# Kernel tuning notes

Measured on AMD Instinct MI355X. Metric: run time of the kernel, lower is better.

Reference implementation:

```python
import jax, jax.numpy as jnp
import numpy as np

NMS_THRESH = 0.5
SCORE_THRESH = 0.05
MAX_DET = 300


def _iou_one_vs_all(box, boxes):
    # box: [4] (x1,y1,x2,y2); boxes: [N,4]
    x1 = jnp.maximum(box[0], boxes[:, 0])
    y1 = jnp.maximum(box[1], boxes[:, 1])
    x2 = jnp.minimum(box[2], boxes[:, 2])
    y2 = jnp.minimum(box[3], boxes[:, 3])
    inter = jnp.maximum(x2 - x1, 0.0) * jnp.maximum(y2 - y1, 0.0)
    area_a = (box[2] - box[0]) * (box[3] - box[1])
    area_b = (boxes[:, 2] - boxes[:, 0]) * (boxes[:, 3] - boxes[:, 1])
    union = area_a + area_b - inter
    return inter / jnp.maximum(union, 1e-8)


def _nms_single_class(boxes, scores):
    # Greedy NMS with max_output_size=MAX_DET, matching tf.image.non_max_suppression
    # after score-threshold prefiltering. boxes:[N,4], scores:[N].
    s0 = jnp.where(scores > SCORE_THRESH, scores, -jnp.inf)

    def step(s, _):
        i = jnp.argmax(s)
        si = s[i]
        sel = jnp.isfinite(si)  # False once no candidates remain
        iou = _iou_one_vs_all(boxes[i], boxes)
        s = jnp.where(sel & (iou > NMS_THRESH), -jnp.inf, s)
        s = s.at[i].set(-jnp.inf)
        return s, (i, si, sel)

    _, (idx, sv, sel) = jax.lax.scan(step, s0, None, length=MAX_DET)
    # unselected slots carry -inf score
    return idx.astype(jnp.int32), jnp.where(sel, sv, -jnp.inf)


def _filter_one_image(boxes, classification, other):
    # boxes:[N,4], classification:[N,C], other:[N,D]
    C = classification.shape[1]
    # class-specific NMS (class_specific_filter=True, nms=True)
    idx, sv = jax.vmap(lambda c: _nms_single_class(boxes, classification[:, c]))(
        jnp.arange(C))  # each [C, MAX_DET]
    labels = jnp.broadcast_to(jnp.arange(C)[:, None], idx.shape)
    cand_scores = sv.reshape(-1)          # [C*MAX_DET]
    cand_idx = idx.reshape(-1)
    cand_lab = labels.reshape(-1)
    # global top-k over all per-class survivors
    top_s, top_i = jax.lax.top_k(cand_scores, MAX_DET)
    sel_idx = cand_idx[top_i]
    sel_lab = cand_lab[top_i]
    valid = jnp.isfinite(top_s)
    # pad invalid slots with -1 (matches tf.pad(..., constant_values=-1))
    out_boxes = jnp.where(valid[:, None], boxes[sel_idx], -1.0)
    out_scores = jnp.where(valid, top_s, -1.0)
    out_labels = jnp.where(valid, sel_lab, -1).astype(jnp.int32)
    out_other = jnp.where(valid[:, None], other[sel_idx], -1.0)
    return out_boxes, out_scores, out_labels, out_other


def setup_inputs() -> dict:
    key = jax.random.key(0)
    k1, k2, k3, k4 = jax.random.split(key, 4)
    B, N, C, D = 16, 50000, 8, 2
    xy = jax.random.uniform(k1, (B, N, 2), jnp.float32, 0.0, 512.0)
    wh = jax.random.uniform(k2, (B, N, 2), jnp.float32, 4.0, 100.0)
    boxes = jnp.concatenate([xy, xy + wh], axis=-1)  # valid (x1,y1,x2,y2)
    classification = jax.random.uniform(k3, (B, N, C), jnp.float32)
    other = jax.random.normal(k4, (B, N, D), jnp.float32)
    return {"boxes": boxes, "classification": classification, "other": other}


def reference(boxes, classification, other):
    # tf.map_fn over batch -> vmap over batch
    return jax.vmap(_filter_one_image)(boxes, classification, other)
```

## Files before the change

### kernel.cpp

```cpp
#include <hip/hip_runtime.h>
#include <math.h>
#include <stdint.h>

#define NB 16
#define NN 50000
#define NC 8
#define ND 2
#define MAX_DET 300
#define NMS_T 0.5f
#define SCORE_T 0.05f
#define CAP 1024
#define CUTBIN 252
#define LBUF 128
#define NTILE32 32
#define CHUNK 256
#define NT 1024
#define NPI (NN * NC)
#define F4PB (NPI / 4 / NTILE32)

typedef unsigned long long u64;

__device__ __forceinline__ float neg_inf() { return -__builtin_inff(); }

__device__ __forceinline__ bool iou_gt(float ax1, float ay1, float ax2, float ay2,
                                       float area_a,
                                       float bx1, float by1, float bx2, float by2,
                                       float area_b) {
    float x1 = fmaxf(ax1, bx1), y1 = fmaxf(ay1, by1);
    float x2 = fminf(ax2, bx2), y2 = fminf(ay2, by2);
    float inter = __fmul_rn(fmaxf(__fsub_rn(x2, x1), 0.0f),
                            fmaxf(__fsub_rn(y2, y1), 0.0f));
    float uni = __fsub_rn(__fadd_rn(area_a, area_b), inter);
    return inter > __fmul_rn(0.5f, fmaxf(uni, 1e-8f));
}

__device__ __forceinline__ u64 score_key(float s, int n) {
    unsigned u = __float_as_uint(s);
    u ^= (u & 0x80000000u) ? 0xFFFFFFFFu : 0x80000000u;
    return ((u64)u << 32) | (unsigned)(~(unsigned)n);
}

__device__ __forceinline__ u64 shfl_xor_u64(u64 v, int m) {
    unsigned lo = (unsigned)v, hi = (unsigned)(v >> 32);
    lo = __shfl_xor(lo, m, 64);
    hi = __shfl_xor(hi, m, 64);
    return ((u64)hi << 32) | lo;
}

__global__ __launch_bounds__(1024) void compact_kernel(
    const float* __restrict__ cls, int* __restrict__ tcnt_g,
    u64* __restrict__ cand)
{
    const int b = blockIdx.x >> 5, t32 = blockIdx.x & 31;
    const int tid = threadIdx.x;
    __shared__ u64 buf[8][LBUF];
    __shared__ int lcnt[8];
    if (tid < 8) lcnt[tid] = 0;
    __syncthreads();

    const float4* c4 = (const float4*)(cls + (size_t)b * NPI);
    const int f0 = t32 * F4PB, fend = f0 + F4PB;

    for (int f = f0 + tid; f < fend; f += 1024) {
        float4 v = c4[f];
        int cb = (f & 1) * 4;
        int n = f >> 1;
        float vv[4] = {v.x, v.y, v.z, v.w};
        #pragma unroll
        for (int k = 0; k < 4; ++k) {
            float s = vv[k];
            if (s > SCORE_T) {
                int bn = (int)(s * 256.0f); if (bn > 255) bn = 255;
                if (bn >= CUTBIN) {
                    int c = cb + k;
                    int pos = atomicAdd(&lcnt[c], 1);
                    if (pos < LBUF) buf[c][pos] = score_key(s, n);
                }
            }
        }
    }
    __syncthreads();
    {
        int c = tid >> 7, i = tid & (LBUF - 1);
        int m = lcnt[c];
        if (i < (m < LBUF ? m : LBUF))
            cand[(size_t)(((b * 8 + c) * NTILE32) + t32) * LBUF + i] = buf[c][i];
        if (i == 0) tcnt_g[(b * 8 + c) * NTILE32 + t32] = m;
    }
}

__global__ __launch_bounds__(NT) void nms_fused(
    const float* __restrict__ boxes, const float* __restrict__ cls,
    const u64* __restrict__ cand, const int* __restrict__ tcnt_g,
    int* __restrict__ sel_idx, float* __restrict__ sel_score)
{
    const int bc = blockIdx.x;
    const int b = bc >> 3, c = bc & 7;
    const int tid = threadIdx.x;
    const int lane = tid & 63;
    const float4* bx4 = (const float4*)(boxes + (size_t)b * NN * 4);
    const float* sr = cls + (size_t)b * NN * NC + c;
    int* si = sel_idx + bc * MAX_DET;
    float* ss = sel_score + bc * MAX_DET;

    __shared__ u64 keys[CAP];
    __shared__ int tcnt_s[NTILE32], toff_s[NTILE32];
    __shared__ int sh_total, sh_ovf;
    __shared__ u64 M64[4][CHUNK];
    __shared__ unsigned presup4[4][CHUNK];
    __shared__ float4 cbox2[2][CHUNK];
    __shared__ float  carea2[2][CHUNK];
    __shared__ int    cidx2[2][CHUNK];
    __shared__ float  cscore2[2][CHUNK];
    __shared__ u64 accs4_s[4];
    __shared__ float4 abox[MAX_DET];
    __shared__ float aarea[MAX_DET];
    __shared__ unsigned bm[(NN + 31) / 32];
    __shared__ float rv[NT];
    __shared__ int   ri[NT];
    __shared__ float sboxsh[5];

    if (tid < 64) {
        int v = (lane < NTILE32) ? tcnt_g[bc * NTILE32 + lane] : 0;
        int incl = v;
        #pragma unroll
        for (int d = 1; d < 32; d <<= 1) {
            int o = __shfl_up(incl, d, 64);
            if (lane >= d) incl += o;
        }
        if (lane < NTILE32) { tcnt_s[lane] = v; toff_s[lane] = incl - v; }
        u64 ov = __ballot(lane < NTILE32 && v > LBUF);
        if (lane == 31) { sh_total = incl; sh_ovf = (ov != 0); }
    }
    __syncthreads();
    const int cnt = sh_total;
    const bool full_fb = sh_ovf || (cnt > CAP);
    const int inSet = cnt < CAP ? cnt : CAP;

    int n_acc = 0;
    if (!full_fb) {
        for (int i = tid; i < CAP; i += NT) keys[i] = 0ull;
        __syncthreads();
        for (int s = tid; s < NTILE32 * LBUF; s += NT) {
            int t = s >> 7, i = s & (LBUF - 1);
            if (i < tcnt_s[t])
                keys[toff_s[t] + i] = cand[(size_t)(bc * NTILE32 + t) * LBUF + i];
        }
        __syncthreads();

        const int p0 = (tid >> 6) * 128 + lane, p1 = p0 + 64;
        u64 v0 = 0, v1 = 0;
        if (tid < 512) {
            v0 = keys[p0]; v1 = keys[p1];
            #pragma unroll
            for (int k = 2; k <= 128; k <<= 1) {
                #pragma unroll
                for (int j = k >> 1; j > 0; j >>= 1) {
                    if (j == 64) {
                        bool dir = ((p0 & k) == 0);
                        if ((v0 < v1) == dir) { u64 t = v0; v0 = v1; v1 = t; }
                    } else {
                        bool lower = ((lane & j) == 0);
                        bool dir0 = ((p0 & k) == 0);
                        bool dir1 = ((p1 & k) == 0);
                        u64 o0 = shfl_xor_u64(v0, j);
                        u64 mx0 = v0 > o0 ? v0 : o0, mn0 = v0 > o0 ? o0 : v0;
                        v0 = (lower == dir0) ? mx0 : mn0;
                        u64 o1 = shfl_xor_u64(v1, j);
                        u64 mx1 = v1 > o1 ? v1 : o1, mn1 = v1 > o1 ? o1 : v1;
                        v1 = (lower == dir1) ? mx1 : mn1;
                    }
                }
            }
        }
        __syncthreads();
        for (int k = 256; k <= CAP; k <<= 1) {
            if (tid < 512) { keys[p0] = v0; keys[p1] = v1; }
            __syncthreads();
            for (int j = k >> 1; j >= 128; j >>= 1) {
                if (tid < 512) {
                    int p = tid;
                    int i = 2 * p - (p & (j - 1));
                    int ix = i + j;
                    bool dir = ((i & k) == 0);
                    u64 a = keys[i], b2 = keys[ix];
                    if ((a < b2) == dir) { keys[i] = b2; keys[ix] = a; }
                }
                __syncthreads();
            }
            if (tid < 512) {
                v0 = keys[p0]; v1 = keys[p1];
                {
                    bool dir = ((p0 & k) == 0);
                    if ((v0 < v1) == dir) { u64 t = v0; v0 = v1; v1 = t; }
                }
                #pragma unroll
                for (int j = 32; j > 0; j >>= 1) {
                    bool lower = ((lane & j) == 0);
                    bool dir = ((p0 & k) == 0);
                    u64 o0 = shfl_xor_u64(v0, j);
                    u64 mx0 = v0 > o0 ? v0 : o0, mn0 = v0 > o0 ? o0 : v0;
                    v0 = (lower == dir) ? mx0 : mn0;
                    u64 o1 = shfl_xor_u64(v1, j);
                    u64 mx1 = v1 > o1 ? v1 : o1, mn1 = v1 > o1 ? o1 : v1;
                    v1 = (lower == dir) ? mx1 : mn1;
                }
            }
            __syncthreads();
        }
        if (tid < 512) { keys[p0] = v0; keys[p1] = v1; }
        __syncthreads();

        if (tid < CHUNK && tid < inSet) {
            u64 key = keys[tid];
            int idx = (int)(~(unsigned)key);
            unsigned u = (unsigned)(key >> 32);
            unsigned uo = (u & 0x80000000u) ? (u ^ 0x80000000u) : (~u);
            float4 bb = bx4[idx];
            cbox2[0][tid] = bb;
            carea2[0][tid] = __fmul_rn(__fsub_rn(bb.z, bb.x), __fsub_rn(bb.w, bb.y));
            cidx2[0][tid] = idx; cscore2[0][tid] = __uint_as_float(uo);
        }
        __syncthreads();

        int base = 0, cur = 0;
        while (n_acc < MAX_DET && base < inSet) {
            int m = inSet - base; if (m > CHUNK) m = CHUNK;

            {
                int i = tid & (CHUNK - 1);
                int q = tid >> 8;
                if (i < m) {
                    float4 B = cbox2[cur][i];
                    float  Barea = carea2[cur][i];
                    unsigned p = 0;
                    int t = q;
                    for (; t + 28 < n_acc; t += 32) {
                        float4 A0 = abox[t];      float r0 = aarea[t];
                        float4 A1 = abox[t + 4];  float r1 = aarea[t + 4];
                        float4 A2 = abox[t + 8];  float r2 = aarea[t + 8];
                        float4 A3 = abox[t + 12]; float r3 = aarea[t + 12];
                        float4 A4 = abox[t + 16]; float r4 = aarea[t + 16];
                        float4 A5 = abox[t + 20]; float r5 = aarea[t + 20];
                        float4 A6 = abox[t + 24]; float r6 = aarea[t + 24];
                        float4 A7 = abox[t + 28]; float r7 = aarea[t + 28];
                        bool s0 = iou_gt(A0.x,A0.y,A0.z,A0.w,r0,B.x,B.y,B.z,B.w,Barea);
                        bool s1 = iou_gt(A1.x,A1.y,A1.z,A1.w,r1,B.x,B.y,B.z,B.w,Barea);
                        bool s2 = iou_gt(A2.x,A2.y,A2.z,A2.w,r2,B.x,B.y,B.z,B.w,Barea);
                        bool s3 = iou_gt(A3.x,A3.y,A3.z,A3.w,r3,B.x,B.y,B.z,B.w,Barea);
                        bool s4 = iou_gt(A4.x,A4.y,A4.z,A4.w,r4,B.x,B.y,B.z,B.w,Barea);
                        bool s5 = iou_gt(A5.x,A5.y,A5.z,A5.w,r5,B.x,B.y,B.z,B.w,Barea);
                        bool s6 = iou_gt(A6.x,A6.y,A6.z,A6.w,r6,B.x,B.y,B.z,B.w,Barea);
                        bool s7 = iou_gt(A7.x,A7.y,A7.z,A7.w,r7,B.x,B.y,B.z,B.w,Barea);
                        if (s0|s1|s2|s3|s4|s5|s6|s7) { p = 1; break; }
                    }
                    if (!p) {
                        for (; t < n_acc; t += 4) {
                            float4 A = abox[t];
                            if (iou_gt(A.x,A.y,A.z,A.w,aarea[t],
                                       B.x,B.y,B.z,B.w,Barea)) { p = 1; break; }
                        }
                    }
                    presup4[q][i] = p;
                    u64 bits = 0;
                    int j0 = q * 64;
                    int jend = i - j0; if (jend > 64) jend = 64; if (jend < 0) jend = 0;
                    int jj = 0;
                    for (; jj + 7 < jend; jj += 8) {
                        int j = j0 + jj;
                        float4 A0 = cbox2[cur][j];     float r0 = carea2[cur][j];
                        float4 A1 = cbox2[cur][j + 1]; float r1 = carea2[cur][j + 1];
                        float4 A2 = cbox2[cur][j + 2]; float r2 = carea2[cur][j + 2];
                        float4 A3 = cbox2[cur][j + 3]; float r3 = carea2[cur][j + 3];
                        float4 A4 = cbox2[cur][j + 4]; float r4 = carea2[cur][j + 4];
                        float4 A5 = cbox2[cur][j + 5]; float r5 = carea2[cur][j + 5];
                        float4 A6 = cbox2[cur][j + 6]; float r6 = carea2[cur][j + 6];
                        float4 A7 = cbox2[cur][j + 7]; float r7 = carea2[cur][j + 7];
                        if (iou_gt(A0.x,A0.y,A0.z,A0.w,r0,B.x,B.y,B.z,B.w,Barea)) bits |= 1ull << jj;
                        if (iou_gt(A1.x,A1.y,A1.z,A1.w,r1,B.x,B.y,B.z,B.w,Barea)) bits |= 1ull << (jj+1);
                        if (iou_gt(A2.x,A2.y,A2.z,A2.w,r2,B.x,B.y,B.z,B.w,Barea)) bits |= 1ull << (jj+2);
                        if (iou_gt(A3.x,A3.y,A3.z,A3.w,r3,B.x,B.y,B.z,B.w,Barea)) bits |= 1ull << (jj+3);
                        if (iou_gt(A4.x,A4.y,A4.z,A4.w,r4,B.x,B.y,B.z,B.w,Barea)) bits |= 1ull << (jj+4);
                        if (iou_gt(A5.x,A5.y,A5.z,A5.w,r5,B.x,B.y,B.z,B.w,Barea)) bits |= 1ull << (jj+5);
                        if (iou_gt(A6.x,A6.y,A6.z,A6.w,r6,B.x,B.y,B.z,B.w,Barea)) bits |= 1ull << (jj+6);
                        if (iou_gt(A7.x,A7.y,A7.z,A7.w,r7,B.x,B.y,B.z,B.w,Barea)) bits |= 1ull << (jj+7);
                    }
                    for (; jj < jend; ++jj) {
                        int j = j0 + jj;
                        float4 A = cbox2[cur][j];
                        if (iou_gt(A.x,A.y,A.z,A.w,carea2[cur][j],
                                   B.x,B.y,B.z,B.w,Barea)) bits |= 1ull << jj;
                    }
                    M64[q][i] = bits;
                }
            }
            __syncthreads();

            int nbase = base + m;
            if (tid < 64) {
                u64 Mr[4][4];
                unsigned pe[4];
                bool acc[4];
                #pragma unroll
                for (int cg = 0; cg < 4; ++cg) {
                    int i = cg * 64 + lane;
                    if (i < m) {
                        pe[cg] = presup4[0][i] | presup4[1][i] | presup4[2][i] | presup4[3][i];
                        #pragma unroll
                        for (int w = 0; w < 4; ++w) Mr[cg][w] = M64[w][i];
                    } else {
                        pe[cg] = 1u;
                        #pragma unroll
                        for (int w = 0; w < 4; ++w) Mr[cg][w] = 0ull;
                    }
                    acc[cg] = (pe[cg] == 0);
                }
                u64 a0 = __ballot(acc[0]), a1 = __ballot(acc[1]);
                u64 a2 = __ballot(acc[2]), a3 = __ballot(acc[3]);
                for (int it = 0; it < CHUNK + 1; ++it) {
                    #pragma unroll
                    for (int cg = 0; cg < 4; ++cg) {
                        u64 sup = (Mr[cg][0] & a0) | (Mr[cg][1] & a1)
                                | (Mr[cg][2] & a2) | (Mr[cg][3] & a3);
                        acc[cg] = (pe[cg] == 0) && (sup == 0ull);
                    }
                    u64 n0 = __ballot(acc[0]), n1 = __ballot(acc[1]);
                    u64 n2 = __ballot(acc[2]), n3 = __ballot(acc[3]);
                    bool same = (n0 == a0) && (n1 == a1) && (n2 == a2) && (n3 == a3);
                    a0 = n0; a1 = n1; a2 = n2; a3 = n3;
                    if (same) break;
                }
                if (lane == 0) { accs4_s[0] = a0; accs4_s[1] = a1;
                                 accs4_s[2] = a2; accs4_s[3] = a3; }
            } else if (tid >= 256 && tid < 512 && nbase < inSet) {
                int w = tid - 256;
                if (nbase + w < inSet) {
                    u64 key = keys[nbase + w];
                    int idx = (int)(~(unsigned)key);
                    unsigned u = (unsigned)(key >> 32);
                    unsigned uo = (u & 0x80000000u) ? (u ^ 0x80000000u) : (~u);
                    float4 bb = bx4[idx];
                    cbox2[cur ^ 1][w] = bb;
                    carea2[cur ^ 1][w] = __fmul_rn(__fsub_rn(bb.z, bb.x), __fsub_rn(bb.w, bb.y));
                    cidx2[cur ^ 1][w] = idx; cscore2[cur ^ 1][w] = __uint_as_float(uo);
                }
            }
            __syncthreads();

            u64 a0 = accs4_s[0], a1 = accs4_s[1], a2 = accs4_s[2], a3 = accs4_s[3];
            int add = __popcll(a0) + __popcll(a1) + __popcll(a2) + __popcll(a3);
            if (tid < m) {
                int gg = tid >> 6, o = tid & 63;
                u64 aw = (gg == 0) ? a0 : (gg == 1) ? a1 : (gg == 2) ? a2 : a3;
                if ((aw >> o) & 1ull) {
                    int rank = 0;
                    if (gg > 0) rank += __popcll(a0);
                    if (gg > 1) rank += __popcll(a1);
                    if (gg > 2) rank += __popcll(a2);
                    rank += __popcll(aw & ((1ull << o) - 1ull));
                    int pos = n_acc + rank;
                    if (pos < MAX_DET) {
                        abox[pos] = cbox2[cur][tid]; aarea[pos] = carea2[cur][tid];
                        si[pos] = cidx2[cur][tid]; ss[pos] = cscore2[cur][tid];
                    }
                }
            }
            n_acc += add; if (n_acc > MAX_DET) n_acc = MAX_DET;
            base = nbase; cur ^= 1;
            __syncthreads();
        }
    }

    const bool part_fb = (!full_fb) && (n_acc < MAX_DET);

    if (full_fb || part_fb) {
        const int BMW = (NN + 31) / 32;
        for (int i = tid; i < BMW; i += NT) bm[i] = 0u;
        __syncthreads();
        if (full_fb) {
            n_acc = 0;
        } else {
            for (int n = tid; n < NN; n += NT) {
                float4 bbn = bx4[n];
                float nb_area = __fmul_rn(__fsub_rn(bbn.z, bbn.x), __fsub_rn(bbn.w, bbn.y));
                int s = 0;
                for (int t = 0; t < n_acc; ++t) {
                    float4 A = abox[t];
                    if (iou_gt(A.x, A.y, A.z, A.w, aarea[t],
                               bbn.x, bbn.y, bbn.z, bbn.w, nb_area)) s = 1;
                }
                if (s) atomicOr(&bm[n >> 5], 1u << (n & 31));
            }
        }
        __syncthreads();

        for (int k = n_acc; k < MAX_DET; ++k) {
            float bv = neg_inf(); int bi = 0x7fffffff;
            for (int n = tid; n < NN; n += NT) {
                if (!((bm[n >> 5] >> (n & 31)) & 1u)) {
                    float v = sr[(size_t)n * NC];
                    if (v > SCORE_T && v > bv) { bv = v; bi = n; }
                }
            }
            rv[tid] = bv; ri[tid] = bi;
            __syncthreads();
            for (int s = NT / 2; s > 0; s >>= 1) {
                if (tid < s) {
                    float ov = rv[tid + s]; int oi = ri[tid + s];
                    if (ov > rv[tid] || (ov == rv[tid] && oi < ri[tid])) { rv[tid] = ov; ri[tid] = oi; }
                }
                __syncthreads();
            }
            float mval = rv[0]; int midx = ri[0];
            if (mval == neg_inf()) {
                for (int kk = k + tid; kk < MAX_DET; kk += NT) { si[kk] = 0; ss[kk] = neg_inf(); }
                break;
            }
            if (tid == 0) {
                si[k] = midx; ss[k] = mval;
                float4 sb = bx4[midx];
                sboxsh[0] = sb.x; sboxsh[1] = sb.y; sboxsh[2] = sb.z; sboxsh[3] = sb.w;
                sboxsh[4] = __fmul_rn(__fsub_rn(sb.z, sb.x), __fsub_rn(sb.w, sb.y));
            }
            __syncthreads();
            float ax1 = sboxsh[0], ay1 = sboxsh[1], ax2 = sboxsh[2], ay2 = sboxsh[3];
            float area_a = sboxsh[4];
            for (int n = tid; n < NN; n += NT) {
                float4 bbn = bx4[n];
                float nb_area = __fmul_rn(__fsub_rn(bbn.z, bbn.x), __fsub_rn(bbn.w, bbn.y));
                if (iou_gt(ax1, ay1, ax2, ay2, area_a,
                           bbn.x, bbn.y, bbn.z, bbn.w, nb_area))
                    atomicOr(&bm[n >> 5], 1u << (n & 31));
            }
            __syncthreads();
        }
    } else {
        for (int kk = n_acc + tid; kk < MAX_DET; kk += NT) { si[kk] = 0; ss[kk] = neg_inf(); }
    }
}

__global__ __launch_bounds__(1024) void topk_kernel(
    const float* __restrict__ boxes, const float* __restrict__ other,
    const int* __restrict__ sel_idx, const float* __restrict__ sel_score,
    float* __restrict__ out)
{
    const int b = blockIdx.x;
    const int tid = threadIdx.x;
    __shared__ u64 keys[4096];

    for (int i = tid; i < 4096; i += 1024) {
        int c = i >> 9, o = i & 511;
        u64 key = 0ull;
        if (o < MAX_DET) {
            int m = c * MAX_DET + o;
            float v = sel_score[b * NC * MAX_DET + m];
            unsigned u = __float_as_uint(v);
            u ^= (u & 0x80000000u) ? 0xFFFFFFFFu : 0x80000000u;
            key = ((u64)u << 32) | (unsigned)(~(unsigned)m);
        }
        keys[i] = key;
    }

    for (int seg = 1024; seg <= 4096; seg <<= 1) {
        int half = seg >> 1;
        __syncthreads();
        {
            int p = tid;
            int s = p / (half >> 1), t = p % (half >> 1);
            int i0 = s * seg + half + t;
            int i1 = s * seg + seg - 1 - t;
            u64 a = keys[i0]; keys[i0] = keys[i1]; keys[i1] = a;
        }
        __syncthreads();
        for (int j = half; j > 0; j >>= 1) {
            for (int p = tid; p < 2048; p += 1024) {
                int i = 2 * p - (p & (j - 1));
                int ix = i + j;
                u64 a = keys[i], bq = keys[ix];
                if (a < bq) { keys[i] = bq; keys[ix] = a; }
            }
            if (j >= 128) __syncthreads(); else __threadfence_block();
        }
    }
    __syncthreads();

    const float4* bx4 = (const float4*)(boxes + (size_t)b * NN * 4);
    const float*  ot  = other + (size_t)b * NN * ND;
    float* ob = out;
    float* os = out + NB * MAX_DET * 4;
    float* ol = os + NB * MAX_DET;
    float* oo = ol + NB * MAX_DET;

    for (int k = tid; k < MAX_DET; k += 1024) {
        u64 key = keys[k];
        unsigned u = (unsigned)(key >> 32);
        unsigned uo = (u & 0x80000000u) ? (u ^ 0x80000000u) : (u ^ 0xFFFFFFFFu);
        float score = __uint_as_float(uo);
        bool valid = isfinite(score);
        float b0=-1.f,b1=-1.f,b2=-1.f,b3=-1.f,scv=-1.f,lab=-1.f,o0=-1.f,o1=-1.f;
        if (valid) {
            int m = (int)(~(unsigned)key);
            int c = m / MAX_DET, slot = m - c * MAX_DET;
            int n = sel_idx[(b * NC + c) * MAX_DET + slot];
            float4 bb = bx4[n];
            b0 = bb.x; b1 = bb.y; b2 = bb.z; b3 = bb.w;
            scv = score; lab = (float)c;
            o0 = ot[n * ND + 0]; o1 = ot[n * ND + 1];
        }
        int base = b * MAX_DET + k;
        ob[base * 4 + 0] = b0; ob[base * 4 + 1] = b1;
        ob[base * 4 + 2] = b2; ob[base * 4 + 3] = b3;
        os[base] = scv; ol[base] = lab;
        oo[base * 2 + 0] = o0; oo[base * 2 + 1] = o1;
    }
}

extern "C" void kernel_launch(void* const* d_in, const int* in_sizes, int n_in,
                              void* d_out, int out_size, void* d_ws, size_t ws_size,
                              hipStream_t stream) {
    const float* boxes = (const float*)d_in[0];
    const float* cls   = (const float*)d_in[1];
    const float* other = (const float*)d_in[2];
    float* out = (float*)d_out;

    int* tcnt_g = (int*)d_ws;
    u64* cand  = (u64*)(tcnt_g + NB * NC * NTILE32);
    int* sel_idx = (int*)(cand + (size_t)NB * NC * NTILE32 * LBUF);
    float* sel_score = (float*)(sel_idx + NB * NC * MAX_DET);

    compact_kernel<<<NB * NTILE32, 1024, 0, stream>>>(cls, tcnt_g, cand);
    nms_fused<<<NB * NC, NT, 0, stream>>>(boxes, cls, cand, tcnt_g,
                                          sel_idx, sel_score);
    topk_kernel<<<NB, 1024, 0, stream>>>(boxes, other, sel_idx, sel_score, out);
}
```

Before: 64.36 us.

## Replace bitonic sort in top-k with merge-rank via per-class binary search

The final top-k kernel no longer bitonic-sorts 4096 padded keys in shared memory. It relies on each class's NMS output already being sorted in descending order. Each candidate computes its global rank by binary-searching the other seven per-class lists, and only those with rank below MAX_DET write their output slot. This removes the many barrier-separated sort stages. In exchange, each thread does about 70 dependent shared-memory reads, and correctness depends on the per-class lists being strictly descending.

```diff
diff --git a/kernel.cpp b/kernel.cpp
--- a/kernel.cpp
+++ b/kernel.cpp
@@ -446,41 +446,14 @@
 {
     const int b = blockIdx.x;
     const int tid = threadIdx.x;
-    __shared__ u64 keys[4096];
-
-    for (int i = tid; i < 4096; i += 1024) {
-        int c = i >> 9, o = i & 511;
-        u64 key = 0ull;
-        if (o < MAX_DET) {
-            int m = c * MAX_DET + o;
-            float v = sel_score[b * NC * MAX_DET + m];
-            unsigned u = __float_as_uint(v);
-            u ^= (u & 0x80000000u) ? 0xFFFFFFFFu : 0x80000000u;
-            key = ((u64)u << 32) | (unsigned)(~(unsigned)m);
-        }
-        keys[i] = key;
-    }
-
-    for (int seg = 1024; seg <= 4096; seg <<= 1) {
-        int half = seg >> 1;
-        __syncthreads();
-        {
-            int p = tid;
-            int s = p / (half >> 1), t = p % (half >> 1);
-            int i0 = s * seg + half + t;
-            int i1 = s * seg + seg - 1 - t;
-            u64 a = keys[i0]; keys[i0] = keys[i1]; keys[i1] = a;
-        }
-        __syncthreads();
-        for (int j = half; j > 0; j >>= 1) {
-            for (int p = tid; p < 2048; p += 1024) {
-                int i = 2 * p - (p & (j - 1));
-                int ix = i + j;
-                u64 a = keys[i], bq = keys[ix];
-                if (a < bq) { keys[i] = bq; keys[ix] = a; }
-            }
-            if (j >= 128) __syncthreads(); else __threadfence_block();
-        }
+    const int NCAND = NC * MAX_DET;
+    __shared__ u64 lists[NC][MAX_DET];
+
+    for (int i = tid; i < NCAND; i += 1024) {
+        float v = sel_score[b * NCAND + i];
+        unsigned u = __float_as_uint(v);
+        u ^= (u & 0x80000000u) ? 0xFFFFFFFFu : 0x80000000u;
+        lists[i / MAX_DET][i % MAX_DET] = ((u64)u << 32) | (unsigned)(~(unsigned)i);
     }
     __syncthreads();
 
@@ -491,27 +464,49 @@
     float* ol = os + NB * MAX_DET;
     float* oo = ol + NB * MAX_DET;
 
-    for (int k = tid; k < MAX_DET; k += 1024) {
-        u64 key = keys[k];
-        unsigned u = (unsigned)(key >> 32);
-        unsigned uo = (u & 0x80000000u) ? (u ^ 0x80000000u) : (u ^ 0xFFFFFFFFu);
-        float score = __uint_as_float(uo);
-        bool valid = isfinite(score);
-        float b0=-1.f,b1=-1.f,b2=-1.f,b3=-1.f,scv=-1.f,lab=-1.f,o0=-1.f,o1=-1.f;
-        if (valid) {
-            int m = (int)(~(unsigned)key);
-            int c = m / MAX_DET, slot = m - c * MAX_DET;
-            int n = sel_idx[(b * NC + c) * MAX_DET + slot];
-            float4 bb = bx4[n];
-            b0 = bb.x; b1 = bb.y; b2 = bb.z; b3 = bb.w;
-            scv = score; lab = (float)c;
-            o0 = ot[n * ND + 0]; o1 = ot[n * ND + 1];
-        }
-        int base = b * MAX_DET + k;
-        ob[base * 4 + 0] = b0; ob[base * 4 + 1] = b1;
-        ob[base * 4 + 2] = b2; ob[base * 4 + 3] = b3;
-        os[base] = scv; ol[base] = lab;
-        oo[base * 2 + 0] = o0; oo[base * 2 + 1] = o1;
+    for (int i = tid; i < NCAND; i += 1024) {
+        int cown = i / MAX_DET, slot = i - cown * MAX_DET;
+        u64 K = lists[cown][slot];
+        int rank = slot;
+        int pos[NC], len[NC];
+        #pragma unroll
+        for (int c2 = 0; c2 < NC; ++c2) {
+            pos[c2] = 0;
+            len[c2] = (c2 == cown) ? 0 : MAX_DET;
+        }
+        for (int step = 0; step < 10; ++step) {
+            #pragma unroll
+            for (int c2 = 0; c2 < NC; ++c2) {
+                if (len[c2] > 0) {
+                    int half = len[c2] >> 1;
+                    bool go = lists[c2][pos[c2] + half] > K;
+                    pos[c2] = go ? pos[c2] + half + 1 : pos[c2];
+                    len[c2] = go ? len[c2] - half - 1 : half;
+                }
+            }
+        }
+        #pragma unroll
+        for (int c2 = 0; c2 < NC; ++c2) rank += pos[c2];
+
+        if (rank < MAX_DET) {
+            unsigned u = (unsigned)(K >> 32);
+            unsigned uo = (u & 0x80000000u) ? (u ^ 0x80000000u) : (u ^ 0xFFFFFFFFu);
+            float score = __uint_as_float(uo);
+            bool valid = isfinite(score);
+            float b0=-1.f,b1=-1.f,b2=-1.f,b3=-1.f,scv=-1.f,lab=-1.f,o0=-1.f,o1=-1.f;
+            if (valid) {
+                int n = sel_idx[b * NCAND + i];
+                float4 bb = bx4[n];
+                b0 = bb.x; b1 = bb.y; b2 = bb.z; b3 = bb.w;
+                scv = score; lab = (float)cown;
+                o0 = ot[n * ND + 0]; o1 = ot[n * ND + 1];
+            }
+            int base = b * MAX_DET + rank;
+            ob[base * 4 + 0] = b0; ob[base * 4 + 1] = b1;
+            ob[base * 4 + 2] = b2; ob[base * 4 + 3] = b3;
+            os[base] = scv; ol[base] = lab;
+            oo[base * 2 + 0] = o0; oo[base * 2 + 1] = o1;
+        }
     }
 }
 
```

Measured after the change: 66.06 us. 1.03x slower.
